# Performance work log

Measured on AMD Instinct MI355X. Metric: run time of the kernel, lower is better.

Reference implementation:

```python
import jax, jax.numpy as jnp
import numpy as np

B, S, D, E = 8, 128, 768, 100

def setup_inputs() -> dict:
    key = jax.random.key(0)
    ks = jax.random.split(key, 7)
    s = 1.0 / np.sqrt(D)  # roughly Linear init scale
    return {
        "x":     jax.random.normal(ks[0], (B, S, D), dtype=jnp.float32),
        "w_lin": jax.random.normal(ks[1], (E, D, D), dtype=jnp.float32) * s,
        "b_lin": jax.random.normal(ks[2], (E, D), dtype=jnp.float32) * s,
        "w1":    jax.random.normal(ks[3], (E, D, D), dtype=jnp.float32) * s,
        "b1":    jax.random.normal(ks[4], (E, D), dtype=jnp.float32) * s,
        "w2":    jax.random.normal(ks[5], (E, D, D), dtype=jnp.float32) * s,
        "b2":    jax.random.normal(ks[6], (E, D), dtype=jnp.float32) * s,
    }

def reference(x, w_lin, b_lin, w1, b1, w2, b2):
    # Torch Linear: y = x @ W.T + b, weights stacked over experts e.
    # Skip branch: [B,S,O,E]
    lin = jnp.einsum('bsd,eod->bsoe', x, w_lin) + b_lin.T[None, None]
    # MLP branch (dropout is identity in eval mode); exact (erf) GELU as nn.GELU default.
    h = jax.nn.gelu(jnp.einsum('bsd,ehd->bseh', x, w1) + b1[None, None], approximate=False)
    mlp = jnp.einsum('bseh,eoh->bsoe', h, w2) + b2.T[None, None]
    # torch.stack([...], dim=-1) -> [B, S, D_out, E]
    return lin + mlp
```

## Files before the change

### kernel.cpp

```cpp
#include <hip/hip_runtime.h>
#include <hip/hip_bf16.h>
#include <cstdint>

typedef __attribute__((ext_vector_type(8))) short short8;
typedef __attribute__((ext_vector_type(4))) float f32x4;
typedef unsigned short u16;
typedef unsigned int u32;

#define Mdim 1024
#define Ddim 768
#define Edim 100
#define DD (Ddim * Ddim)
#define NW8 7372800

__device__ __forceinline__ u16 f2bf(float f) {
  u32 u = __builtin_bit_cast(u32, f);
  u += 0x7fffu + ((u >> 16) & 1u);
  return (u16)(u >> 16);
}
__device__ __forceinline__ float bf2f(u16 h) {
  return __builtin_bit_cast(float, ((u32)h) << 16);
}
__device__ __forceinline__ u32 pack2(float a, float b) {
  return (u32)f2bf(a) | ((u32)f2bf(b) << 16);
}

__device__ __forceinline__ float gelu_f(float v) {
  float v2 = v * v;
  float wv = v * (2.30220795f + 0.10294322f * v2);
  float ew = __builtin_amdgcn_exp2f(wv);
  return v - v * __builtin_amdgcn_rcpf(ew + 1.0f);
}

#define GLL16(gsrc, ldst)                                                        \
  __builtin_amdgcn_global_load_lds(                                             \
      (const __attribute__((address_space(1))) u32*)(gsrc),                     \
      (__attribute__((address_space(3))) u32*)(ldst), 16, 0, 0)

#define VM8 asm volatile("s_waitcnt vmcnt(8)" ::: "memory")
#define VM0 asm volatile("s_waitcnt vmcnt(0)" ::: "memory")
#define LGKM0 asm volatile("s_waitcnt lgkmcnt(0)" ::: "memory")
#define RAW_BAR                                                                  \
  do {                                                                           \
    __builtin_amdgcn_s_barrier();                                                \
    asm volatile("" ::: "memory");                                               \
  } while (0)

__device__ __forceinline__ void cvt8(const float* __restrict__ s, u16* __restrict__ d) {
  const float4 f0 = *(const float4*)(s);
  const float4 f1 = *(const float4*)(s + 4);
  uint4 v;
  v.x = pack2(f0.x, f0.y); v.y = pack2(f0.z, f0.w);
  v.z = pack2(f1.x, f1.y); v.w = pack2(f1.z, f1.w);
  *(uint4*)(d) = v;
}

__global__ __launch_bounds__(256) void k_prep(const float* __restrict__ x,
                                              u16* __restrict__ xb,
                                              const float* __restrict__ w1,
                                              u16* __restrict__ w1b) {
  const int tid = blockIdx.x * 256 + threadIdx.x;
  if (tid < (Mdim * Ddim) / 8) cvt8(x + (size_t)tid * 8, xb + (size_t)tid * 8);
  for (int i = tid; i < NW8; i += 2048 * 256)
    cvt8(w1 + (size_t)i * 8, w1b + (size_t)i * 8);
}

__global__ __launch_bounds__(256) void k_prep2(const float* __restrict__ wl,
                                               u16* __restrict__ wlb,
                                               const float* __restrict__ w2,
                                               u16* __restrict__ w2b) {
  const int tid = blockIdx.x * 256 + threadIdx.x;
  for (int i = tid; i < NW8; i += 2048 * 256) {
    cvt8(wl + (size_t)i * 8, wlb + (size_t)i * 8);
    cvt8(w2 + (size_t)i * 8, w2b + (size_t)i * 8);
  }
}

template <int NT>
__device__ __forceinline__ void gemm8(const u16* __restrict__ A0,
                                      const u16* __restrict__ A1,
                                      const u16* __restrict__ B0,
                                      const u16* __restrict__ B1,
                                      u16* lds, f32x4 (&acc)[8][4], const int t) {
  const int w = t >> 6, l = t & 63;
  const int wr = (w >> 2) << 7;
  const int wc = (w & 3) << 6;
  const int lr = l & 15, c4 = l >> 4, r7 = l & 7;
  const int sl0 = ((c4 ^ r7) << 3);
  const int sl1 = (((4 | c4) ^ r7) << 3);
  const size_t soff = (size_t)((w << 5) + (l >> 3)) * Ddim + (((l & 7) ^ (l >> 3)) << 3);

  auto stage_op = [&](const u16* src, int buf, int isB, int kk) {
    u16* d = lds + (buf << 15) + (isB << 14) + (w << 11);
    const u16* s = src + soff + (kk << 6);
#pragma unroll
    for (int i = 0; i < 4; ++i)
      GLL16(s + (size_t)(i << 3) * Ddim, d + (i << 9));
  };
  auto stage = [&](int tt, int isB) {
    const int buf = tt & 1;
    if (NT == 24 && tt >= 12) stage_op(isB ? B1 : A1, buf, isB, tt - 12);
    else                      stage_op(isB ? B0 : A0, buf, isB, tt);
  };

  short8 af[8], bf0[4], bf1[4];
  auto rdA = [&](int buf, int half) {
    const u16* ab = lds + (buf << 15) + (wr + (half << 6) + lr) * 64;
#pragma unroll
    for (int m = 0; m < 4; ++m) {
      af[m * 2]     = *(const short8*)(ab + (m << 10) + sl0);
      af[m * 2 + 1] = *(const short8*)(ab + (m << 10) + sl1);
    }
  };
  auto rdB = [&](int buf, int half, short8 (&bfh)[4]) {
    const u16* bb = lds + (buf << 15) + 16384 + (wc + (half << 5) + lr) * 64;
#pragma unroll
    for (int n = 0; n < 2; ++n) {
      bfh[n * 2]     = *(const short8*)(bb + (n << 10) + sl0);
      bfh[n * 2 + 1] = *(const short8*)(bb + (n << 10) + sl1);
    }
  };
  auto q = [&](int mh, int nh, short8 (&bfh)[4]) {
    __builtin_amdgcn_s_setprio(1);
#pragma unroll
    for (int m = 0; m < 4; ++m)
#pragma unroll
      for (int n = 0; n < 2; ++n) {
        f32x4 c = acc[mh * 4 + m][nh * 2 + n];
        c = __builtin_amdgcn_mfma_f32_16x16x32_bf16(af[m * 2],     bfh[n * 2],     c, 0, 0, 0);
        c = __builtin_amdgcn_mfma_f32_16x16x32_bf16(af[m * 2 + 1], bfh[n * 2 + 1], c, 0, 0, 0);
        acc[mh * 4 + m][nh * 2 + n] = c;
      }
    __builtin_amdgcn_s_setprio(0);
  };

  stage(0, 1); stage(0, 0);
  stage(1, 1); stage(1, 0);
  VM8;
  RAW_BAR;

#pragma unroll 2
  for (int T = 0; T < NT - 2; ++T) {
    const int buf = T & 1;
    rdB(buf, 0, bf0); rdB(buf, 1, bf1); rdA(buf, 0);
    RAW_BAR; q(0, 0, bf0); RAW_BAR;
    stage(T + 2, 1);
    RAW_BAR; q(0, 1, bf1); RAW_BAR;
    rdA(buf, 1);
    RAW_BAR; q(1, 1, bf1); RAW_BAR;
    stage(T + 2, 0);
    VM8;
    RAW_BAR; q(1, 0, bf0); RAW_BAR;
  }
  {
    const int buf = (NT - 2) & 1;
    rdB(buf, 0, bf0); rdB(buf, 1, bf1); rdA(buf, 0);
    RAW_BAR; q(0, 0, bf0); RAW_BAR;
    RAW_BAR; q(0, 1, bf1); RAW_BAR;
    rdA(buf, 1);
    RAW_BAR; q(1, 1, bf1); RAW_BAR;
    VM0;
    RAW_BAR; q(1, 0, bf0); RAW_BAR;
  }
  {
    const int buf = (NT - 1) & 1;
    rdB(buf, 0, bf0); rdB(buf, 1, bf1); rdA(buf, 0);
    RAW_BAR; q(0, 0, bf0); RAW_BAR;
    RAW_BAR; q(0, 1, bf1); RAW_BAR;
    rdA(buf, 1);
    RAW_BAR; q(1, 1, bf1); RAW_BAR;
    q(1, 0, bf0);
  }
}

template <bool GELU>
__device__ __forceinline__ void epi_store(f32x4 (&acc)[8][4], const float* bias,
                                          u16* lds, u16* gout, int m_base, int n_base,
                                          const int t) {
  const int w = t >> 6, l = t & 63;
  const int lr = l & 15, c4 = l >> 4;
  u16* reg = lds + (w << 13);

  LGKM0;
  __builtin_amdgcn_sched_barrier(0);
  RAW_BAR;

  float bv[4];
#pragma unroll
  for (int nf = 0; nf < 4; ++nf) bv[nf] = bias[(nf << 4) + lr];

#pragma unroll
  for (int mf = 0; mf < 8; ++mf) {
#pragma unroll
    for (int nf = 0; nf < 4; ++nf) {
      const int slot = (nf << 1) + (lr >> 3);
      const int bis = (lr & 7);
#pragma unroll
      for (int j = 0; j < 4; ++j) {
        float v = acc[mf][nf][j] + bv[nf];
        if (GELU) v = gelu_f(v);
        const int row = (mf << 4) + (c4 << 2) + j;
        reg[row * 64 + ((slot ^ (row & 7)) << 3) + bis] = f2bf(v);
      }
    }
  }
  const int g = l >> 3;
  const int phys = ((l & 7) ^ g) << 3;
#pragma unroll
  for (int r = 0; r < 16; ++r) {
    const int row = (r << 3) + g;
    short8 v = *(const short8*)(reg + row * 64 + phys);
    *(short8*)(gout + (size_t)(m_base + row) * Ddim + n_base + ((l & 7) << 3)) = v;
  }
}

__device__ __forceinline__ void decode8(int bid, int& e, int& m0, int& n0) {
  const int s = (bid & 7) * 150 + (bid >> 3);
  e = s / 12;
  const int r = s % 12;
  m0 = (r & 3) << 8;
  n0 = (r >> 2) << 8;
}

__global__ __launch_bounds__(512, 2) void k_h10(const u16* __restrict__ xb,
                                                const u16* __restrict__ w1b,
                                                const float* __restrict__ b1,
                                                u16* __restrict__ hout) {
  __shared__ __align__(16) u16 lds[65536];
  int e, m0, n0;
  decode8(blockIdx.x, e, m0, n0);
  const int t = threadIdx.x;
  f32x4 acc[8][4] = {};
  gemm8<12>(xb + (size_t)m0 * Ddim, nullptr,
            w1b + (size_t)e * DD + (size_t)n0 * Ddim, nullptr, lds, acc, t);

  const int w = t >> 6;
  const int wr = (w >> 2) << 7, wc = (w & 3) << 6;
  epi_store<true>(acc, b1 + (size_t)e * Ddim + n0 + wc, lds,
                  hout + (size_t)e * Mdim * Ddim, m0 + wr, n0 + wc, t);
}

__global__ __launch_bounds__(512, 2) void k_out10(const u16* __restrict__ xb,
                                                  const u16* __restrict__ hbuf,
                                                  const u16* __restrict__ wlb,
                                                  const float* __restrict__ b_lin,
                                                  const u16* __restrict__ w2b,
                                                  const float* __restrict__ b2,
                                                  u16* __restrict__ tout) {
  __shared__ __align__(16) u16 lds[65536];
  int e, m0, n0;
  decode8(blockIdx.x, e, m0, n0);
  const int t = threadIdx.x;
  f32x4 acc[8][4] = {};
  gemm8<24>(xb + (size_t)m0 * Ddim,
            hbuf + (size_t)e * Mdim * Ddim + (size_t)m0 * Ddim,
            wlb + (size_t)e * DD + (size_t)n0 * Ddim,
            w2b + (size_t)e * DD + (size_t)n0 * Ddim, lds, acc, t);

  const int w = t >> 6, l = t & 63;
  const int wr = (w >> 2) << 7, wc = (w & 3) << 6;
  const int lr = l & 15;
  const float* bm = b2 + (size_t)e * Ddim + n0 + wc;
#pragma unroll
  for (int nf = 0; nf < 4; ++nf) {
    const float bmv = bm[(nf << 4) + lr];
#pragma unroll
    for (int mf = 0; mf < 8; ++mf)
#pragma unroll
      for (int j = 0; j < 4; ++j) acc[mf][nf][j] += bmv;
  }
  epi_store<false>(acc, b_lin + (size_t)e * Ddim + n0 + wc, lds,
                   tout + (size_t)e * Mdim * Ddim, m0 + wr, n0 + wc, t);
}

__global__ __launch_bounds__(256) void k_tr_bf(const u16* __restrict__ tbuf,
                                               float* __restrict__ out) {
  __shared__ __align__(16) u16 tile[100 * 260];
  const int t = threadIdx.x;
  const size_t MD = (size_t)Mdim * Ddim;
  const size_t md0 = (size_t)blockIdx.x * 256;
#pragma unroll
  for (int p = 0; p < 25; ++p) {
    const int e = p * 4 + (t >> 6);
    const int c = (t & 63) * 4;
    uint2 v = *(const uint2*)(tbuf + (size_t)e * MD + md0 + c);
    *(uint2*)(&tile[e * 260 + c]) = v;
  }
  __syncthreads();
  const size_t obase = md0 * 100;
#pragma unroll 5
  for (int i = 0; i < 100; ++i) {
    const int flat = t + i * 256;
    const int mo = (int)(((u32)flat * 5243u) >> 19);
    const int e = flat - mo * 100;
    out[obase + flat] = bf2f(tile[e * 260 + mo]);
  }
}

__global__ void k_cvt(const float* __restrict__ x, u16* __restrict__ xb) {
  size_t i = ((size_t)blockIdx.x * 256 + threadIdx.x) * 4;
  float4 v = *(const float4*)(x + i);
  uint2 r;
  r.x = pack2(v.x, v.y);
  r.y = pack2(v.z, v.w);
  *(uint2*)(xb + i) = r;
}

__device__ __forceinline__ void gemm_phase_f32(const u16* __restrict__ Ag,
                                               const float* __restrict__ Wg,
                                               u16* As, u16* Bs, f32x4 (&acc)[4][4], int t) {
  const int w = t >> 6, l = t & 63;
  const int lrow = l & 15, lk = (l >> 4) << 3;
  const int wr = ((w >> 1) << 6), wc = ((w & 1) << 6);
  for (int kt = 0; kt < Ddim; kt += 32) {
#pragma unroll
    for (int i = 0; i < 2; ++i) {
      GLL16(Ag + (size_t)((w << 5) + (i << 4) + (l >> 2)) * Ddim + kt + ((l & 3) << 3),
            As + (((w << 5) + (i << 4)) << 5));
    }
    {
      const int r = t >> 1, c = (t & 1) << 4;
      const float* src = Wg + (size_t)r * Ddim + kt + c;
      const float4 f0 = *(const float4*)(src);
      const float4 f1 = *(const float4*)(src + 4);
      const float4 f2 = *(const float4*)(src + 8);
      const float4 f3 = *(const float4*)(src + 12);
      uint4 v0, v1;
      v0.x = pack2(f0.x, f0.y); v0.y = pack2(f0.z, f0.w);
      v0.z = pack2(f1.x, f1.y); v0.w = pack2(f1.z, f1.w);
      v1.x = pack2(f2.x, f2.y); v1.y = pack2(f2.z, f2.w);
      v1.z = pack2(f3.x, f3.y); v1.w = pack2(f3.z, f3.w);
      *(uint4*)(&Bs[r * 32 + c]) = v0;
      *(uint4*)(&Bs[r * 32 + c + 8]) = v1;
    }
    __syncthreads();
    short8 af[4], bfr[4];
#pragma unroll
    for (int f = 0; f < 4; ++f) {
      af[f]  = *(const short8*)(&As[(wr + f * 16 + lrow) * 32 + lk]);
      bfr[f] = *(const short8*)(&Bs[(wc + f * 16 + lrow) * 32 + lk]);
    }
#pragma unroll
    for (int fm = 0; fm < 4; ++fm)
#pragma unroll
      for (int fn = 0; fn < 4; ++fn)
        acc[fm][fn] = __builtin_amdgcn_mfma_f32_16x16x32_bf16(af[fm], bfr[fn], acc[fm][fn], 0, 0, 0);
    __syncthreads();
  }
}

__global__ __launch_bounds__(256) void k_h2(const u16* __restrict__ xb,
                                            const float* __restrict__ w1,
                                            const float* __restrict__ b1,
                                            u16* __restrict__ hout, int e_base) {
  __shared__ __align__(16) u16 As[128 * 32];
  __shared__ __align__(16) u16 Bs[128 * 32];
  const int el = blockIdx.x / 48, r = blockIdx.x % 48;
  const int m0 = (r / 6) * 128, n0 = (r % 6) * 128;
  const int e = e_base + el;
  const int t = threadIdx.x, l = t & 63, wv = t >> 6;
  const int wr = (wv >> 1) * 64, wc = (wv & 1) * 64, lrow = l & 15;
  f32x4 acc[4][4] = {};
  gemm_phase_f32(xb + (size_t)m0 * Ddim, w1 + (size_t)e * DD + (size_t)n0 * Ddim, As, Bs, acc, t);
  const float* bias = b1 + (size_t)e * Ddim + n0;
  u16* hb = hout + (size_t)el * Mdim * Ddim;
#pragma unroll
  for (int fm = 0; fm < 4; ++fm) {
    const int mb = m0 + wr + fm * 16 + ((l >> 4) << 2);
#pragma unroll
    for (int fn = 0; fn < 4; ++fn) {
      const int nc = wc + fn * 16 + lrow;
      const float bv = bias[nc];
#pragma unroll
      for (int j = 0; j < 4; ++j) {
        float v = acc[fm][fn][j] + bv;
        v = 0.5f * v * (1.0f + erff(v * 0.7071067811865475f));
        hb[(size_t)(mb + j) * Ddim + n0 + nc] = f2bf(v);
      }
    }
  }
}

__global__ __launch_bounds__(256) void k_out2(
    const u16* __restrict__ xb, const u16* __restrict__ hbuf,
    const float* __restrict__ wl, const float* __restrict__ b_lin,
    const float* __restrict__ w2, const float* __restrict__ b2,
    float* __restrict__ out, int e_base) {
  __shared__ __align__(16) u16 As[128 * 32];
  __shared__ __align__(16) u16 Bs[128 * 32];
  const int el = blockIdx.x / 48, r = blockIdx.x % 48;
  const int m0 = (r / 6) * 128, n0 = (r % 6) * 128;
  const int e = e_base + el;
  const int t = threadIdx.x, l = t & 63, wv = t >> 6;
  const int wr = (wv >> 1) * 64, wc = (wv & 1) * 64, lrow = l & 15;
  f32x4 acc[4][4] = {};
  gemm_phase_f32(xb + (size_t)m0 * Ddim, wl + (size_t)e * DD + (size_t)n0 * Ddim, As, Bs, acc, t);
  gemm_phase_f32(hbuf + (size_t)el * Mdim * Ddim + (size_t)m0 * Ddim,
                 w2 + (size_t)e * DD + (size_t)n0 * Ddim, As, Bs, acc, t);
  const float* bl = b_lin + (size_t)e * Ddim + n0;
  const float* bm = b2 + (size_t)e * Ddim + n0;
#pragma unroll
  for (int fm = 0; fm < 4; ++fm) {
    const int mb = m0 + wr + fm * 16 + ((l >> 4) << 2);
#pragma unroll
    for (int fn = 0; fn < 4; ++fn) {
      const int nc = wc + fn * 16 + lrow;
      const float bv = bl[nc] + bm[nc];
#pragma unroll
      for (int j = 0; j < 4; ++j)
        out[((size_t)(mb + j) * Ddim + n0 + nc) * Edim + e] = acc[fm][fn][j] + bv;
    }
  }
}

extern "C" void kernel_launch(void* const* d_in, const int* in_sizes, int n_in,
                              void* d_out, int out_size, void* d_ws, size_t ws_size,
                              hipStream_t stream) {
  const float* x     = (const float*)d_in[0];
  const float* w_lin = (const float*)d_in[1];
  const float* b_lin = (const float*)d_in[2];
  const float* w1    = (const float*)d_in[3];
  const float* b1    = (const float*)d_in[4];
  const float* w2    = (const float*)d_in[5];
  const float* b2    = (const float*)d_in[6];
  float* out = (float*)d_out;

  const size_t MD = (size_t)Mdim * Ddim;
  const size_t xb_b = MD * 2;
  const size_t w_b  = (size_t)Edim * DD * 2;
  const size_t h_b  = (size_t)Edim * MD * 2;
  const size_t tb_b = h_b;

  char* base = (char*)d_ws;

  if (ws_size >= xb_b + 3 * w_b + h_b + tb_b) {
    u16* xb   = (u16*)base;
    u16* w1b  = (u16*)(base + xb_b);
    u16* wlb  = (u16*)(base + xb_b + w_b);
    u16* w2b  = (u16*)(base + xb_b + 2 * w_b);
    u16* hbuf = (u16*)(base + xb_b + 3 * w_b);
    u16* tbuf = (u16*)(base + xb_b + 3 * w_b + h_b);
    k_prep<<<dim3(2048), dim3(256), 0, stream>>>(x, xb, w1, w1b);
    k_h10<<<dim3(1200), dim3(512), 0, stream>>>(xb, w1b, b1, hbuf);
    k_prep2<<<dim3(2048), dim3(256), 0, stream>>>(w_lin, wlb, w2, w2b);
    k_out10<<<dim3(1200), dim3(512), 0, stream>>>(xb, hbuf, wlb, b_lin, w2b, b2, tbuf);
    k_tr_bf<<<dim3((u32)(MD / 256)), dim3(256), 0, stream>>>(tbuf, out);
  } else {
    u16* xb = (u16*)base;
    k_cvt<<<dim3((u32)(MD / 1024)), dim3(256), 0, stream>>>(x, xb);
    size_t avail = ws_size > xb_b ? ws_size - xb_b : 0;
    int EC = (int)(avail / (MD * 2));
    if (EC < 1) EC = 1;
    if (EC > Edim) EC = Edim;
    u16* hbuf = (u16*)(base + xb_b);
    for (int e0 = 0; e0 < Edim; e0 += EC) {
      int ne = (Edim - e0) < EC ? (Edim - e0) : EC;
      k_h2<<<dim3(ne * 48), dim3(256), 0, stream>>>(xb, w1, b1, hbuf, e0);
      k_out2<<<dim3(ne * 48), dim3(256), 0, stream>>>(xb, hbuf, w_lin, b_lin, w2, b2,
                                                      out, e0);
    }
  }
}
```

Measured before the change: 735.6 us.

## Load A operand directly from global into registers, stage only B in LDS

The GEMM main loop now fetches the A (activation) fragments straight from global memory into registers, prefetched one half-tile ahead. Only the B (weight) tile is still staged through LDS with double buffering, which halves LDS traffic and the LDS footprint per buffer. The vmcnt waits are retuned to fit the new mix of outstanding loads, and the epilogue gains a full vmcnt wait. The trade-off is more register pressure and A reads that are less coalesced and repeated across the four column-waves, which may raise global or L2 traffic.

```diff
diff --git a/kernel.cpp b/kernel.cpp
--- a/kernel.cpp
+++ b/kernel.cpp
@@ -37,7 +37,7 @@
       (const __attribute__((address_space(1))) u32*)(gsrc),                     \
       (__attribute__((address_space(3))) u32*)(ldst), 16, 0, 0)
 
-#define VM8 asm volatile("s_waitcnt vmcnt(8)" ::: "memory")
+#define VM(n) asm volatile("s_waitcnt vmcnt(" #n ")" ::: "memory")
 #define VM0 asm volatile("s_waitcnt vmcnt(0)" ::: "memory")
 #define LGKM0 asm volatile("s_waitcnt lgkmcnt(0)" ::: "memory")
 #define RAW_BAR                                                                  \
@@ -77,11 +77,11 @@
 }
 
 template <int NT>
-__device__ __forceinline__ void gemm8(const u16* __restrict__ A0,
-                                      const u16* __restrict__ A1,
-                                      const u16* __restrict__ B0,
-                                      const u16* __restrict__ B1,
-                                      u16* lds, f32x4 (&acc)[8][4], const int t) {
+__device__ __forceinline__ void gemm8r(const u16* __restrict__ A0_,
+                                       const u16* __restrict__ A1_,
+                                       const u16* __restrict__ B0,
+                                       const u16* __restrict__ B1,
+                                       u16* lds, f32x4 (&acc)[8][4], const int t) {
   const int w = t >> 6, l = t & 63;
   const int wr = (w >> 2) << 7;
   const int wc = (w & 3) << 6;
@@ -90,37 +90,34 @@
   const int sl1 = (((4 | c4) ^ r7) << 3);
   const size_t soff = (size_t)((w << 5) + (l >> 3)) * Ddim + (((l & 7) ^ (l >> 3)) << 3);
 
-  auto stage_op = [&](const u16* src, int buf, int isB, int kk) {
-    u16* d = lds + (buf << 15) + (isB << 14) + (w << 11);
+  auto stageB = [&](int tt) {
+    const u16* src = (NT == 24 && tt >= 12) ? B1 : B0;
+    const int kk = (NT == 24 && tt >= 12) ? tt - 12 : tt;
+    u16* d = lds + ((tt & 1) << 14) + (w << 11);
     const u16* s = src + soff + (kk << 6);
 #pragma unroll
     for (int i = 0; i < 4; ++i)
       GLL16(s + (size_t)(i << 3) * Ddim, d + (i << 9));
   };
-  auto stage = [&](int tt, int isB) {
-    const int buf = tt & 1;
-    if (NT == 24 && tt >= 12) stage_op(isB ? B1 : A1, buf, isB, tt - 12);
-    else                      stage_op(isB ? B0 : A0, buf, isB, tt);
-  };
-
-  short8 af[8], bf0[4], bf1[4];
-  auto rdA = [&](int buf, int half) {
-    const u16* ab = lds + (buf << 15) + (wr + (half << 6) + lr) * 64;
+  auto loadA = [&](int tt, int half, short8 (&af)[8]) {
+    const u16* src = (NT == 24 && tt >= 12) ? A1_ : A0_;
+    const int kk = (NT == 24 && tt >= 12) ? tt - 12 : tt;
+    const u16* base = src + (size_t)(wr + (half << 6) + lr) * Ddim + (kk << 6) + (c4 << 3);
 #pragma unroll
     for (int m = 0; m < 4; ++m) {
-      af[m * 2]     = *(const short8*)(ab + (m << 10) + sl0);
-      af[m * 2 + 1] = *(const short8*)(ab + (m << 10) + sl1);
+      af[m * 2]     = *(const short8*)(base + (size_t)(m << 4) * Ddim);
+      af[m * 2 + 1] = *(const short8*)(base + (size_t)(m << 4) * Ddim + 32);
     }
   };
   auto rdB = [&](int buf, int half, short8 (&bfh)[4]) {
-    const u16* bb = lds + (buf << 15) + 16384 + (wc + (half << 5) + lr) * 64;
+    const u16* bb = lds + (buf << 14) + (wc + (half << 5) + lr) * 64;
 #pragma unroll
     for (int n = 0; n < 2; ++n) {
       bfh[n * 2]     = *(const short8*)(bb + (n << 10) + sl0);
       bfh[n * 2 + 1] = *(const short8*)(bb + (n << 10) + sl1);
     }
   };
-  auto q = [&](int mh, int nh, short8 (&bfh)[4]) {
+  auto q = [&](int mh, int nh, short8 (&af)[8], short8 (&bfh)[4]) {
     __builtin_amdgcn_s_setprio(1);
 #pragma unroll
     for (int m = 0; m < 4; ++m)
@@ -134,42 +131,45 @@
     __builtin_amdgcn_s_setprio(0);
   };
 
-  stage(0, 1); stage(0, 0);
-  stage(1, 1); stage(1, 0);
-  VM8;
+  short8 af0[8], af1[8], bf0[4], bf1[4];
+
+  stageB(0); stageB(1);
+  loadA(0, 0, af0);
+  VM(12);
   RAW_BAR;
 
 #pragma unroll 2
   for (int T = 0; T < NT - 2; ++T) {
     const int buf = T & 1;
-    rdB(buf, 0, bf0); rdB(buf, 1, bf1); rdA(buf, 0);
-    RAW_BAR; q(0, 0, bf0); RAW_BAR;
-    stage(T + 2, 1);
-    RAW_BAR; q(0, 1, bf1); RAW_BAR;
-    rdA(buf, 1);
-    RAW_BAR; q(1, 1, bf1); RAW_BAR;
-    stage(T + 2, 0);
-    VM8;
-    RAW_BAR; q(1, 0, bf0); RAW_BAR;
+    loadA(T, 1, af1);
+    rdB(buf, 0, bf0); rdB(buf, 1, bf1);
+    RAW_BAR; LGKM0; q(0, 0, af0, bf0); RAW_BAR;
+    stageB(T + 2);
+    RAW_BAR; q(0, 1, af0, bf1); RAW_BAR;
+    loadA(T + 1, 0, af0);
+    RAW_BAR; q(1, 1, af1, bf1); RAW_BAR;
+    VM(28);
+    RAW_BAR; q(1, 0, af1, bf0); RAW_BAR;
   }
   {
     const int buf = (NT - 2) & 1;
-    rdB(buf, 0, bf0); rdB(buf, 1, bf1); rdA(buf, 0);
-    RAW_BAR; q(0, 0, bf0); RAW_BAR;
-    RAW_BAR; q(0, 1, bf1); RAW_BAR;
-    rdA(buf, 1);
-    RAW_BAR; q(1, 1, bf1); RAW_BAR;
-    VM0;
-    RAW_BAR; q(1, 0, bf0); RAW_BAR;
+    loadA(NT - 2, 1, af1);
+    rdB(buf, 0, bf0); rdB(buf, 1, bf1);
+    RAW_BAR; LGKM0; q(0, 0, af0, bf0); RAW_BAR;
+    RAW_BAR; q(0, 1, af0, bf1); RAW_BAR;
+    loadA(NT - 1, 0, af0);
+    RAW_BAR; q(1, 1, af1, bf1); RAW_BAR;
+    VM(24);
+    RAW_BAR; q(1, 0, af1, bf0); RAW_BAR;
   }
   {
     const int buf = (NT - 1) & 1;
-    rdB(buf, 0, bf0); rdB(buf, 1, bf1); rdA(buf, 0);
-    RAW_BAR; q(0, 0, bf0); RAW_BAR;
-    RAW_BAR; q(0, 1, bf1); RAW_BAR;
-    rdA(buf, 1);
-    RAW_BAR; q(1, 1, bf1); RAW_BAR;
-    q(1, 0, bf0);
+    loadA(NT - 1, 1, af1);
+    rdB(buf, 0, bf0); rdB(buf, 1, bf1);
+    RAW_BAR; LGKM0; q(0, 0, af0, bf0); RAW_BAR;
+    RAW_BAR; q(0, 1, af0, bf1); RAW_BAR;
+    RAW_BAR; q(1, 1, af1, bf1); RAW_BAR;
+    q(1, 0, af1, bf0);
   }
 }
 
@@ -181,6 +181,7 @@
   const int lr = l & 15, c4 = l >> 4;
   u16* reg = lds + (w << 13);
 
+  VM0;
   LGKM0;
   __builtin_amdgcn_sched_barrier(0);
   RAW_BAR;
@@ -222,7 +223,7 @@
   n0 = (r >> 2) << 8;
 }
 
-__global__ __launch_bounds__(512, 2) void k_h10(const u16* __restrict__ xb,
+__global__ __launch_bounds__(512, 2) void k_h11(const u16* __restrict__ xb,
                                                 const u16* __restrict__ w1b,
                                                 const float* __restrict__ b1,
                                                 u16* __restrict__ hout) {
@@ -231,8 +232,8 @@
   decode8(blockIdx.x, e, m0, n0);
   const int t = threadIdx.x;
   f32x4 acc[8][4] = {};
-  gemm8<12>(xb + (size_t)m0 * Ddim, nullptr,
-            w1b + (size_t)e * DD + (size_t)n0 * Ddim, nullptr, lds, acc, t);
+  gemm8r<12>(xb + (size_t)m0 * Ddim, nullptr,
+             w1b + (size_t)e * DD + (size_t)n0 * Ddim, nullptr, lds, acc, t);
 
   const int w = t >> 6;
   const int wr = (w >> 2) << 7, wc = (w & 3) << 6;
@@ -240,7 +241,7 @@
                   hout + (size_t)e * Mdim * Ddim, m0 + wr, n0 + wc, t);
 }
 
-__global__ __launch_bounds__(512, 2) void k_out10(const u16* __restrict__ xb,
+__global__ __launch_bounds__(512, 2) void k_out11(const u16* __restrict__ xb,
                                                   const u16* __restrict__ hbuf,
                                                   const u16* __restrict__ wlb,
                                                   const float* __restrict__ b_lin,
@@ -252,10 +253,10 @@
   decode8(blockIdx.x, e, m0, n0);
   const int t = threadIdx.x;
   f32x4 acc[8][4] = {};
-  gemm8<24>(xb + (size_t)m0 * Ddim,
-            hbuf + (size_t)e * Mdim * Ddim + (size_t)m0 * Ddim,
-            wlb + (size_t)e * DD + (size_t)n0 * Ddim,
-            w2b + (size_t)e * DD + (size_t)n0 * Ddim, lds, acc, t);
+  gemm8r<24>(xb + (size_t)m0 * Ddim,
+             hbuf + (size_t)e * Mdim * Ddim + (size_t)m0 * Ddim,
+             wlb + (size_t)e * DD + (size_t)n0 * Ddim,
+             w2b + (size_t)e * DD + (size_t)n0 * Ddim, lds, acc, t);
 
   const int w = t >> 6, l = t & 63;
   const int wr = (w >> 2) << 7, wc = (w & 3) << 6;
@@ -441,9 +442,9 @@
     u16* hbuf = (u16*)(base + xb_b + 3 * w_b);
     u16* tbuf = (u16*)(base + xb_b + 3 * w_b + h_b);
     k_prep<<<dim3(2048), dim3(256), 0, stream>>>(x, xb, w1, w1b);
-    k_h10<<<dim3(1200), dim3(512), 0, stream>>>(xb, w1b, b1, hbuf);
+    k_h11<<<dim3(1200), dim3(512), 0, stream>>>(xb, w1b, b1, hbuf);
     k_prep2<<<dim3(2048), dim3(256), 0, stream>>>(w_lin, wlb, w2, w2b);
-    k_out10<<<dim3(1200), dim3(512), 0, stream>>>(xb, hbuf, wlb, b_lin, w2b, b2, tbuf);
+    k_out11<<<dim3(1200), dim3(512), 0, stream>>>(xb, hbuf, wlb, b_lin, w2b, b2, tbuf);
     k_tr_bf<<<dim3((u32)(MD / 256)), dim3(256), 0, stream>>>(tbuf, out);
   } else {
     u16* xb = (u16*)base;
```

Result: slower. 1.248 ms (+69.7%).
